# Optimization experiments

Measured on AMD Instinct MI355X. Metric: run time of the kernel, lower is better.

The kernel has to match this reference:

```python
import jax, jax.numpy as jnp
import numpy as np

FP8_MAX = 448.0  # max normal for float8_e4m3fn
BLOCK = 128


def setup_inputs() -> dict:
    key = jax.random.key(0)
    k1, k2, k3 = jax.random.split(key, 3)
    B, S, D_IN, D_OUT = 2, 2048, 4096, 8192
    x = jax.random.normal(k1, (B, S, D_IN), dtype=jnp.float32)
    # stored weight is fp8_e4m3fn; materialize as f32 values that are exactly fp8-representable
    w = jax.random.normal(k2, (D_OUT, D_IN), dtype=jnp.float32)
    weight = w.astype(jnp.float8_e4m3fn).astype(jnp.float32)
    # positive per-(128x128)-block dequant scales
    weight_scale_inv = (
        jax.random.uniform(k3, (D_OUT // BLOCK, D_IN // BLOCK), dtype=jnp.float32) * 0.05 + 0.005
    )
    return {"x": x, "weight": weight, "weight_scale_inv": weight_scale_inv}


def _quantize_per_token(x2d):
    # x2d: [M, K] -> fp8 values + [M, 1] f32 scale
    amax = jnp.clip(jnp.max(jnp.abs(x2d), axis=-1, keepdims=True), min=1e-12)
    x_scale = (amax / FP8_MAX).astype(jnp.float32)
    x_fp8 = (x2d / x_scale).astype(jnp.float8_e4m3fn)
    return x_fp8, x_scale


def _dequantize_weight(weight, weight_scale_inv):
    # weight: [O, K] (fp8-representable f32), scales: [O/B, K/B]
    O, K = weight.shape
    w_fp8 = weight.astype(jnp.float8_e4m3fn).astype(jnp.float32)
    wb = w_fp8.reshape(O // BLOCK, BLOCK, K // BLOCK, BLOCK)
    wb = wb * weight_scale_inv[:, None, :, None]
    return wb.reshape(O, K)


def reference(x, weight, weight_scale_inv):
    orig_shape = x.shape
    x2d = x.reshape(-1, orig_shape[-1])  # [M, K], M > 1 path
    x_fp8, x_scale = _quantize_per_token(x2d)
    # block-scaled fp8 GEMM: y[m,n] = x_scale[m] * sum_k x_fp8[m,k] * w_fp8[n,k] * s[n//B,k//B]
    w_deq = _dequantize_weight(weight, weight_scale_inv)  # [O, K]
    y = jnp.einsum("mk,ok->mo", x_fp8.astype(jnp.float32), w_deq) * x_scale
    return y.reshape(*orig_shape[:-1], weight.shape[0])
```

## Files before the change

kernel.cpp:

```cpp
#include <hip/hip_runtime.h>

typedef float f32x4  __attribute__((ext_vector_type(4)));
typedef float f32x16 __attribute__((ext_vector_type(16)));
typedef int   i32x4  __attribute__((ext_vector_type(4)));
typedef int   i32x8  __attribute__((ext_vector_type(8)));

#define AS1 __attribute__((address_space(1)))
#define AS3 __attribute__((address_space(3)))

__global__ __launch_bounds__(256) void quant_x_fp8_kernel(
    const float* __restrict__ x, unsigned char* __restrict__ x8,
    float* __restrict__ xs, int K) {
  int m = blockIdx.x;
  int t = threadIdx.x;
  const f32x4* src = (const f32x4*)(x + (size_t)m * K + t * 16);
  f32x4 v[4];
  float am = 0.0f;
#pragma unroll
  for (int i = 0; i < 4; ++i) {
    v[i] = src[i];
#pragma unroll
    for (int j = 0; j < 4; ++j) am = fmaxf(am, __builtin_fabsf(v[i][j]));
  }
#pragma unroll
  for (int off = 32; off >= 1; off >>= 1)
    am = fmaxf(am, __shfl_xor(am, off, 64));
  __shared__ float red[4];
  int wv = t >> 6, lane = t & 63;
  if (lane == 0) red[wv] = am;
  __syncthreads();
  am = fmaxf(fmaxf(red[0], red[1]), fmaxf(red[2], red[3]));
  am = fmaxf(am, 1e-12f);
  float sc = am / 448.0f;
  if (t == 0) xs[m] = sc;
  i32x4 out;
#pragma unroll
  for (int i = 0; i < 4; ++i) {
    float q0 = v[i][0] / sc, q1 = v[i][1] / sc;
    float q2 = v[i][2] / sc, q3 = v[i][3] / sc;
    int p = __builtin_amdgcn_cvt_pk_fp8_f32(q0, q1, 0, false);
    p = __builtin_amdgcn_cvt_pk_fp8_f32(q2, q3, p, true);
    out[i] = p;
  }
  *(i32x4*)(x8 + (size_t)m * K + t * 16) = out;
}

__global__ __launch_bounds__(256) void quant_w_fp8_kernel(
    const float* __restrict__ w, unsigned char* __restrict__ w8) {
  size_t idx = (size_t)blockIdx.x * 256 + threadIdx.x;
  const f32x4* src = (const f32x4*)w + idx * 4;
  i32x4 out;
#pragma unroll
  for (int i = 0; i < 4; ++i) {
    f32x4 v = src[i];
    int p = __builtin_amdgcn_cvt_pk_fp8_f32(v[0], v[1], 0, false);
    p = __builtin_amdgcn_cvt_pk_fp8_f32(v[2], v[3], p, true);
    out[i] = p;
  }
  ((i32x4*)w8)[idx] = out;
}

__global__ __launch_bounds__(512, 1) void gemm_mxfp8_kernel(
    const unsigned char* __restrict__ A8,
    const unsigned char* __restrict__ W8,
    const float* __restrict__ xs,
    const float* __restrict__ wsinv,
    float* __restrict__ Y,
    int M, int N, int K) {
  const int KB = K >> 7;

  int bid = blockIdx.x, nwg = gridDim.x;
  int wg = (bid & 7) * (nwg >> 3) + (bid >> 3);
  int mt = M >> 8;
  int bm = wg & (mt - 1);
  int bn = wg / mt;
  int m0 = bm << 8, n0 = bn << 7;

  __shared__ __align__(16) char lds[147456];

  const int tid = threadIdx.x, wv = tid >> 6, lane = tid & 63;
  const int wr = wv >> 1, wc = wv & 1;
  const int l31 = lane & 31, hi2 = lane >> 5;
  const int salt = l31 & 7;

  const int sL0 = ((hi2 * 2 + 0) ^ salt) << 4;
  const int sH0 = ((hi2 * 2 + 1) ^ salt) << 4;
  const int sL1 = ((4 + hi2 * 2 + 0) ^ salt) << 4;
  const int sH1 = ((4 + hi2 * 2 + 1) ^ salt) << 4;

  const int aRow = (wr * 64 + l31) * 128;
  const int bRow = (wc * 64 + l31) * 128;
  const int aL0 = aRow + sL0, aH0 = aRow + sH0;
  const int aL1 = aRow + sL1, aH1 = aRow + sH1;
  const int bL0 = bRow + sL0, bH0 = bRow + sH0;
  const int bL1 = bRow + sL1, bH1 = bRow + sH1;

  const int stgD = tid << 4;
  const int rIdx = tid >> 3;
  const int cSrc = ((tid & 7) ^ ((tid >> 3) & 7)) << 4;
  const size_t rowB = (size_t)K;
  const size_t g64 = 64 * rowB;
  const char* pA = (const char*)A8 + (size_t)(m0 + rIdx) * rowB + cSrc;
  const char* pB = (const char*)W8 + (size_t)(n0 + rIdx) * rowB + cSrc;

  const float* wsv = wsinv + (size_t)bn * KB;

  f32x16 acc[2][2];
#pragma unroll
  for (int i = 0; i < 2; ++i)
#pragma unroll
    for (int j = 0; j < 2; ++j) acc[i][j] = (f32x16)0.0f;

  i32x8 af[2], bf[2][2];

#define GL(SRC, DST)                                                           \
  __builtin_amdgcn_global_load_lds((const AS1 void*)(SRC), (AS3 void*)(DST),   \
                                   16, 0, 0)
#define STG_A(COND, SB, SRC)                                                   \
  if (COND) {                                                                  \
    const char* s_ = (SRC);                                                    \
    char* d_ = lds + (SB) + stgD;                                              \
    GL(s_, d_);                                                                \
    GL(s_ + g64, d_ + 8192);                                                   \
    GL(s_ + 2 * g64, d_ + 16384);                                              \
    GL(s_ + 3 * g64, d_ + 24576);                                              \
  }
#define STG_B(COND, SB, SRC)                                                   \
  if (COND) {                                                                  \
    const char* s_ = (SRC);                                                    \
    char* d_ = lds + (SB) + stgD;                                              \
    GL(s_, d_);                                                                \
    GL(s_ + g64, d_ + 8192);                                                   \
  }

#define RD_A(RB, MJ)                                                           \
  {                                                                            \
    const char* p_ = lds + (RB) + (MJ) * 4096;                                 \
    i32x4 lo0 = *(const i32x4*)(p_ + aL0);                                     \
    i32x4 hi0 = *(const i32x4*)(p_ + aH0);                                     \
    i32x4 lo1 = *(const i32x4*)(p_ + aL1);                                     \
    i32x4 hi1 = *(const i32x4*)(p_ + aH1);                                     \
    af[0] = __builtin_shufflevector(lo0, hi0, 0, 1, 2, 3, 4, 5, 6, 7);         \
    af[1] = __builtin_shufflevector(lo1, hi1, 0, 1, 2, 3, 4, 5, 6, 7);         \
  }
#define RD_Bn(RB, NJ)                                                          \
  {                                                                            \
    const char* p_ = lds + (RB) + (NJ) * 4096;                                 \
    i32x4 lo0 = *(const i32x4*)(p_ + bL0);                                     \
    i32x4 hi0 = *(const i32x4*)(p_ + bH0);                                     \
    i32x4 lo1 = *(const i32x4*)(p_ + bL1);                                     \
    i32x4 hi1 = *(const i32x4*)(p_ + bH1);                                     \
    bf[NJ][0] = __builtin_shufflevector(lo0, hi0, 0, 1, 2, 3, 4, 5, 6, 7);     \
    bf[NJ][1] = __builtin_shufflevector(lo1, hi1, 0, 1, 2, 3, 4, 5, 6, 7);     \
  }

#define MMFn(MJ, NJ, R_)                                                       \
  {                                                                            \
    _Pragma("unroll") for (int q = 0; q < 16; ++q)                             \
        acc[MJ][NJ][q] *= (R_);                                                \
    acc[MJ][NJ] = __builtin_amdgcn_mfma_scale_f32_32x32x64_f8f6f4(             \
        af[0], bf[NJ][0], acc[MJ][NJ], 0, 0, 0, 0x7f7f7f7f, 0, 0x7f7f7f7f);    \
    acc[MJ][NJ] = __builtin_amdgcn_mfma_scale_f32_32x32x64_f8f6f4(             \
        af[1], bf[NJ][1], acc[MJ][NJ], 0, 0, 0, 0x7f7f7f7f, 0, 0x7f7f7f7f);    \
  }

  STG_A(true, 0, pA);
  STG_B(true, 98304, pB);
  STG_A(true, 32768, pA + 128);
  STG_B(true, 114688, pB + 128);
  asm volatile("s_waitcnt vmcnt(6)" ::: "memory");
  __builtin_amdgcn_s_barrier();

  int rdA = 0;
  int stA = 65536;
  int rdB = 98304;
  int stB = 131072;
  const char* pAs = pA + 256;
  const char* pBs = pB + 256;
  float sp_ = wsv[0];

#define TILE(T, G, VM)                                                         \
  {                                                                            \
    float sc_ = wsv[(T)];                                                      \
    float r_ = sp_ / sc_;                                                      \
    RD_A(rdA, 0);                                                              \
    RD_Bn(rdB, 0);                                                             \
    __builtin_amdgcn_s_setprio(1);                                             \
    MMFn(0, 0, r_);                                                            \
    __builtin_amdgcn_s_setprio(0);                                             \
    STG_A(G, stA, pAs);                                                        \
    STG_B(G, stB, pBs);                                                        \
    RD_Bn(rdB, 1);                                                             \
    __builtin_amdgcn_s_setprio(1);                                             \
    MMFn(0, 1, r_);                                                            \
    __builtin_amdgcn_s_setprio(0);                                             \
    RD_A(rdA, 1);                                                              \
    __builtin_amdgcn_s_setprio(1);                                             \
    MMFn(1, 0, r_);                                                            \
    MMFn(1, 1, r_);                                                            \
    __builtin_amdgcn_s_setprio(0);                                             \
    sp_ = sc_;                                                                 \
    asm volatile("s_waitcnt " VM ::: "memory");                                \
    __builtin_amdgcn_s_barrier();                                              \
    rdA = (rdA == 65536) ? 0 : rdA + 32768;                                    \
    stA = (stA == 65536) ? 0 : stA + 32768;                                    \
    rdB = (rdB == 131072) ? 98304 : rdB + 16384;                               \
    stB = (stB == 131072) ? 98304 : stB + 16384;                               \
    pAs += 128;                                                                \
    pBs += 128;                                                                \
  }

#pragma unroll 1
  for (int t = 0; t < KB - 2; ++t) {
    TILE(t, true, "vmcnt(6)")
  }
  TILE(KB - 2, false, "vmcnt(0)")
  TILE(KB - 1, false, "vmcnt(0)")

#undef TILE
#undef MMFn
#undef RD_Bn
#undef RD_A
#undef STG_B
#undef STG_A
#undef GL

  const float sl_ = sp_;
#pragma unroll
  for (int mj = 0; mj < 2; ++mj)
#pragma unroll
    for (int nj = 0; nj < 2; ++nj) {
      int col = n0 + wc * 64 + nj * 32 + l31;
#pragma unroll
      for (int q = 0; q < 4; ++q) {
        int row0 = m0 + wr * 64 + mj * 32 + q * 8 + hi2 * 4;
        f32x4 sv = *(const f32x4*)(xs + row0);
#pragma unroll
        for (int j = 0; j < 4; ++j)
          Y[(size_t)(row0 + j) * N + col] = acc[mj][nj][q * 4 + j] * sv[j] * sl_;
      }
    }
}

extern "C" void kernel_launch(void* const* d_in, const int* in_sizes, int n_in,
                              void* d_out, int out_size, void* d_ws, size_t ws_size,
                              hipStream_t stream) {
  const float* x     = (const float*)d_in[0];
  const float* w     = (const float*)d_in[1];
  const float* wsinv = (const float*)d_in[2];
  float* y = (float*)d_out;

  const int K = 4096;
  const int M = in_sizes[0] / K;
  const int N = in_sizes[1] / K;

  unsigned char* x8 = (unsigned char*)d_ws;
  float* xs = (float*)((char*)d_ws + (size_t)M * K);
  unsigned char* w8 =
      (unsigned char*)d_ws + (size_t)M * K + (size_t)M * 4;

  quant_x_fp8_kernel<<<M, 256, 0, stream>>>(x, x8, xs, K);
  quant_w_fp8_kernel<<<(int)(((size_t)N * K / 16 + 255) / 256), 256, 0,
                       stream>>>(w, w8);

  dim3 grid((M / 256) * (N / 128));
  gemm_mxfp8_kernel<<<grid, 512, 0, stream>>>(x8, w8, xs, wsinv, y, M, N, K);
}
```

Before: 226.7 us.

## Shrink GEMM LDS pipeline to double-buffered A and single-buffered B

Replaces the 3-stage A / 3-stage B LDS ring buffer with a 2-stage A buffer and a single B buffer. B is now read fully up front and refilled after a mid-tile barrier. This cuts LDS use from 144KB to 80KB and raises the launch-bounds occupancy hint, which lets the kernel rely on more resident waves instead of deep prefetch. In exchange, prefetch depth drops, waits become vmcnt(0) every tile, and an extra barrier is added per k-block. Latency exposure may rise, and at 80KB of LDS per 512-thread block occupancy may still be limited.

```diff
diff --git a/kernel.cpp b/kernel.cpp
--- a/kernel.cpp
+++ b/kernel.cpp
@@ -60,7 +60,7 @@
   ((i32x4*)w8)[idx] = out;
 }
 
-__global__ __launch_bounds__(512, 1) void gemm_mxfp8_kernel(
+__global__ __launch_bounds__(512, 4) void gemm_mxfp8_kernel(
     const unsigned char* __restrict__ A8,
     const unsigned char* __restrict__ W8,
     const float* __restrict__ xs,
@@ -76,7 +76,7 @@
   int bn = wg / mt;
   int m0 = bm << 8, n0 = bn << 7;
 
-  __shared__ __align__(16) char lds[147456];
+  __shared__ __align__(16) char lds[81920];
 
   const int tid = threadIdx.x, wv = tid >> 6, lane = tid & 63;
   const int wr = wv >> 1, wc = wv & 1;
@@ -143,15 +143,15 @@
     af[0] = __builtin_shufflevector(lo0, hi0, 0, 1, 2, 3, 4, 5, 6, 7);         \
     af[1] = __builtin_shufflevector(lo1, hi1, 0, 1, 2, 3, 4, 5, 6, 7);         \
   }
-#define RD_Bn(RB, NJ)                                                          \
-  {                                                                            \
-    const char* p_ = lds + (RB) + (NJ) * 4096;                                 \
+#define RD_B(BR)                                                               \
+  _Pragma("unroll") for (int nj = 0; nj < 2; ++nj) {                           \
+    const char* p_ = lds + (BR) + nj * 4096;                                   \
     i32x4 lo0 = *(const i32x4*)(p_ + bL0);                                     \
     i32x4 hi0 = *(const i32x4*)(p_ + bH0);                                     \
     i32x4 lo1 = *(const i32x4*)(p_ + bL1);                                     \
     i32x4 hi1 = *(const i32x4*)(p_ + bH1);                                     \
-    bf[NJ][0] = __builtin_shufflevector(lo0, hi0, 0, 1, 2, 3, 4, 5, 6, 7);     \
-    bf[NJ][1] = __builtin_shufflevector(lo1, hi1, 0, 1, 2, 3, 4, 5, 6, 7);     \
+    bf[nj][0] = __builtin_shufflevector(lo0, hi0, 0, 1, 2, 3, 4, 5, 6, 7);     \
+    bf[nj][1] = __builtin_shufflevector(lo1, hi1, 0, 1, 2, 3, 4, 5, 6, 7);     \
   }
 
 #define MMFn(MJ, NJ, R_)                                                       \
@@ -165,32 +165,28 @@
   }
 
   STG_A(true, 0, pA);
-  STG_B(true, 98304, pB);
-  STG_A(true, 32768, pA + 128);
-  STG_B(true, 114688, pB + 128);
-  asm volatile("s_waitcnt vmcnt(6)" ::: "memory");
+  STG_B(true, 65536, pB);
+  asm volatile("s_waitcnt vmcnt(0)" ::: "memory");
   __builtin_amdgcn_s_barrier();
 
-  int rdA = 0;
-  int stA = 65536;
-  int rdB = 98304;
-  int stB = 131072;
-  const char* pAs = pA + 256;
-  const char* pBs = pB + 256;
+  int rdA = 0, stA = 32768;
+  const char* pAs = pA + 128;
+  const char* pBs = pB + 128;
   float sp_ = wsv[0];
 
-#define TILE(T, G, VM)                                                         \
+#define TILE(T, G)                                                             \
   {                                                                            \
     float sc_ = wsv[(T)];                                                      \
     float r_ = sp_ / sc_;                                                      \
+    RD_B(65536);                                                               \
     RD_A(rdA, 0);                                                              \
-    RD_Bn(rdB, 0);                                                             \
+    STG_A(G, stA, pAs);                                                        \
     __builtin_amdgcn_s_setprio(1);                                             \
     MMFn(0, 0, r_);                                                            \
     __builtin_amdgcn_s_setprio(0);                                             \
-    STG_A(G, stA, pAs);                                                        \
-    STG_B(G, stB, pBs);                                                        \
-    RD_Bn(rdB, 1);                                                             \
+    asm volatile("s_waitcnt lgkmcnt(0)" ::: "memory");                         \
+    __builtin_amdgcn_s_barrier();                                              \
+    STG_B(G, 65536, pBs);                                                      \
     __builtin_amdgcn_s_setprio(1);                                             \
     MMFn(0, 1, r_);                                                            \
     __builtin_amdgcn_s_setprio(0);                                             \
@@ -200,26 +196,23 @@
     MMFn(1, 1, r_);                                                            \
     __builtin_amdgcn_s_setprio(0);                                             \
     sp_ = sc_;                                                                 \
-    asm volatile("s_waitcnt " VM ::: "memory");                                \
+    asm volatile("s_waitcnt vmcnt(0)" ::: "memory");                           \
     __builtin_amdgcn_s_barrier();                                              \
-    rdA = (rdA == 65536) ? 0 : rdA + 32768;                                    \
-    stA = (stA == 65536) ? 0 : stA + 32768;                                    \
-    rdB = (rdB == 131072) ? 98304 : rdB + 16384;                               \
-    stB = (stB == 131072) ? 98304 : stB + 16384;                               \
+    rdA ^= 32768;                                                              \
+    stA ^= 32768;                                                              \
     pAs += 128;                                                                \
     pBs += 128;                                                                \
   }
 
 #pragma unroll 1
-  for (int t = 0; t < KB - 2; ++t) {
-    TILE(t, true, "vmcnt(6)")
-  }
-  TILE(KB - 2, false, "vmcnt(0)")
-  TILE(KB - 1, false, "vmcnt(0)")
+  for (int t = 0; t < KB - 1; ++t) {
+    TILE(t, true)
+  }
+  TILE(KB - 1, false)
 
 #undef TILE
 #undef MMFn
-#undef RD_Bn
+#undef RD_B
 #undef RD_A
 #undef STG_B
 #undef STG_A
```

New measurement: 824.0 us. +263.6%, slower.

## Halve workgroup to 4 waves with 128x64 per-wave tiles and triple-buffered LDS

Applied to the files above, without the earlier changes.

The GEMM now runs 256 threads (4 waves) per workgroup instead of 512. Each wave computes a 128x64 output tile (4x2 MFMA blocks) instead of 64x64, which raises register reuse of the B fragments per LDS read. The LDS layout changes to three interleaved A+B stage buffers of 48KB each, and the global-to-LDS load issue is spread across the tile's MFMA groups. The trade-off is more accumulator registers per wave and half as many waves to hide latency.

```diff
diff --git a/kernel.cpp b/kernel.cpp
--- a/kernel.cpp
+++ b/kernel.cpp
@@ -60,7 +60,7 @@
   ((i32x4*)w8)[idx] = out;
 }
 
-__global__ __launch_bounds__(512, 1) void gemm_mxfp8_kernel(
+__global__ __launch_bounds__(256, 1) void gemm_mxfp8_kernel(
     const unsigned char* __restrict__ A8,
     const unsigned char* __restrict__ W8,
     const float* __restrict__ xs,
@@ -88,7 +88,7 @@
   const int sL1 = ((4 + hi2 * 2 + 0) ^ salt) << 4;
   const int sH1 = ((4 + hi2 * 2 + 1) ^ salt) << 4;
 
-  const int aRow = (wr * 64 + l31) * 128;
+  const int aRow = (wr * 128 + l31) * 128;
   const int bRow = (wc * 64 + l31) * 128;
   const int aL0 = aRow + sL0, aH0 = aRow + sH0;
   const int aL1 = aRow + sL1, aH1 = aRow + sH1;
@@ -97,17 +97,17 @@
 
   const int stgD = tid << 4;
   const int rIdx = tid >> 3;
-  const int cSrc = ((tid & 7) ^ ((tid >> 3) & 7)) << 4;
+  const int cSrc = ((tid & 7) ^ (rIdx & 7)) << 4;
   const size_t rowB = (size_t)K;
-  const size_t g64 = 64 * rowB;
+  const size_t g32 = 32 * rowB;
   const char* pA = (const char*)A8 + (size_t)(m0 + rIdx) * rowB + cSrc;
   const char* pB = (const char*)W8 + (size_t)(n0 + rIdx) * rowB + cSrc;
 
   const float* wsv = wsinv + (size_t)bn * KB;
 
-  f32x16 acc[2][2];
-#pragma unroll
-  for (int i = 0; i < 2; ++i)
+  f32x16 acc[4][2];
+#pragma unroll
+  for (int i = 0; i < 4; ++i)
 #pragma unroll
     for (int j = 0; j < 2; ++j) acc[i][j] = (f32x16)0.0f;
 
@@ -121,16 +121,22 @@
     const char* s_ = (SRC);                                                    \
     char* d_ = lds + (SB) + stgD;                                              \
     GL(s_, d_);                                                                \
-    GL(s_ + g64, d_ + 8192);                                                   \
-    GL(s_ + 2 * g64, d_ + 16384);                                              \
-    GL(s_ + 3 * g64, d_ + 24576);                                              \
+    GL(s_ + g32, d_ + 4096);                                                   \
+    GL(s_ + 2 * g32, d_ + 8192);                                               \
+    GL(s_ + 3 * g32, d_ + 12288);                                              \
+    GL(s_ + 4 * g32, d_ + 16384);                                              \
+    GL(s_ + 5 * g32, d_ + 20480);                                              \
+    GL(s_ + 6 * g32, d_ + 24576);                                              \
+    GL(s_ + 7 * g32, d_ + 28672);                                              \
   }
 #define STG_B(COND, SB, SRC)                                                   \
   if (COND) {                                                                  \
     const char* s_ = (SRC);                                                    \
-    char* d_ = lds + (SB) + stgD;                                              \
+    char* d_ = lds + (SB) + 32768 + stgD;                                      \
     GL(s_, d_);                                                                \
-    GL(s_ + g64, d_ + 8192);                                                   \
+    GL(s_ + g32, d_ + 4096);                                                   \
+    GL(s_ + 2 * g32, d_ + 8192);                                               \
+    GL(s_ + 3 * g32, d_ + 12288);                                              \
   }
 
 #define RD_A(RB, MJ)                                                           \
@@ -143,15 +149,15 @@
     af[0] = __builtin_shufflevector(lo0, hi0, 0, 1, 2, 3, 4, 5, 6, 7);         \
     af[1] = __builtin_shufflevector(lo1, hi1, 0, 1, 2, 3, 4, 5, 6, 7);         \
   }
-#define RD_Bn(RB, NJ)                                                          \
-  {                                                                            \
-    const char* p_ = lds + (RB) + (NJ) * 4096;                                 \
+#define RD_B(RB)                                                               \
+  _Pragma("unroll") for (int nj = 0; nj < 2; ++nj) {                           \
+    const char* p_ = lds + (RB) + 32768 + nj * 4096;                           \
     i32x4 lo0 = *(const i32x4*)(p_ + bL0);                                     \
     i32x4 hi0 = *(const i32x4*)(p_ + bH0);                                     \
     i32x4 lo1 = *(const i32x4*)(p_ + bL1);                                     \
     i32x4 hi1 = *(const i32x4*)(p_ + bH1);                                     \
-    bf[NJ][0] = __builtin_shufflevector(lo0, hi0, 0, 1, 2, 3, 4, 5, 6, 7);     \
-    bf[NJ][1] = __builtin_shufflevector(lo1, hi1, 0, 1, 2, 3, 4, 5, 6, 7);     \
+    bf[nj][0] = __builtin_shufflevector(lo0, hi0, 0, 1, 2, 3, 4, 5, 6, 7);     \
+    bf[nj][1] = __builtin_shufflevector(lo1, hi1, 0, 1, 2, 3, 4, 5, 6, 7);     \
   }
 
 #define MMFn(MJ, NJ, R_)                                                       \
@@ -165,16 +171,13 @@
   }
 
   STG_A(true, 0, pA);
-  STG_B(true, 98304, pB);
-  STG_A(true, 32768, pA + 128);
-  STG_B(true, 114688, pB + 128);
-  asm volatile("s_waitcnt vmcnt(6)" ::: "memory");
+  STG_B(true, 0, pB);
+  STG_A(true, 49152, pA + 128);
+  STG_B(true, 49152, pB + 128);
+  asm volatile("s_waitcnt vmcnt(12)" ::: "memory");
   __builtin_amdgcn_s_barrier();
 
-  int rdA = 0;
-  int stA = 65536;
-  int rdB = 98304;
-  int stB = 131072;
+  int rdT = 0, stT = 98304;
   const char* pAs = pA + 256;
   const char* pBs = pB + 256;
   float sp_ = wsv[0];
@@ -183,43 +186,48 @@
   {                                                                            \
     float sc_ = wsv[(T)];                                                      \
     float r_ = sp_ / sc_;                                                      \
-    RD_A(rdA, 0);                                                              \
-    RD_Bn(rdB, 0);                                                             \
+    RD_B(rdT);                                                                 \
+    RD_A(rdT, 0);                                                              \
     __builtin_amdgcn_s_setprio(1);                                             \
     MMFn(0, 0, r_);                                                            \
-    __builtin_amdgcn_s_setprio(0);                                             \
-    STG_A(G, stA, pAs);                                                        \
-    STG_B(G, stB, pBs);                                                        \
-    RD_Bn(rdB, 1);                                                             \
-    __builtin_amdgcn_s_setprio(1);                                             \
     MMFn(0, 1, r_);                                                            \
     __builtin_amdgcn_s_setprio(0);                                             \
-    RD_A(rdA, 1);                                                              \
+    STG_A(G, stT, pAs);                                                        \
+    RD_A(rdT, 1);                                                              \
     __builtin_amdgcn_s_setprio(1);                                             \
     MMFn(1, 0, r_);                                                            \
     MMFn(1, 1, r_);                                                            \
+    __builtin_amdgcn_s_setprio(0);                                             \
+    STG_B(G, stT, pBs);                                                        \
+    RD_A(rdT, 2);                                                              \
+    __builtin_amdgcn_s_setprio(1);                                             \
+    MMFn(2, 0, r_);                                                            \
+    MMFn(2, 1, r_);                                                            \
+    __builtin_amdgcn_s_setprio(0);                                             \
+    RD_A(rdT, 3);                                                              \
+    __builtin_amdgcn_s_setprio(1);                                             \
+    MMFn(3, 0, r_);                                                            \
+    MMFn(3, 1, r_);                                                            \
     __builtin_amdgcn_s_setprio(0);                                             \
     sp_ = sc_;                                                                 \
     asm volatile("s_waitcnt " VM ::: "memory");                                \
     __builtin_amdgcn_s_barrier();                                              \
-    rdA = (rdA == 65536) ? 0 : rdA + 32768;                                    \
-    stA = (stA == 65536) ? 0 : stA + 32768;                                    \
-    rdB = (rdB == 131072) ? 98304 : rdB + 16384;                               \
-    stB = (stB == 131072) ? 98304 : stB + 16384;                               \
+    rdT = (rdT == 98304) ? 0 : rdT + 49152;                                    \
+    stT = (stT == 98304) ? 0 : stT + 49152;                                    \
     pAs += 128;                                                                \
     pBs += 128;                                                                \
   }
 
 #pragma unroll 1
   for (int t = 0; t < KB - 2; ++t) {
-    TILE(t, true, "vmcnt(6)")
+    TILE(t, true, "vmcnt(12)")
   }
   TILE(KB - 2, false, "vmcnt(0)")
   TILE(KB - 1, false, "vmcnt(0)")
 
 #undef TILE
 #undef MMFn
-#undef RD_Bn
+#undef RD_B
 #undef RD_A
 #undef STG_B
 #undef STG_A
@@ -227,13 +235,13 @@
 
   const float sl_ = sp_;
 #pragma unroll
-  for (int mj = 0; mj < 2; ++mj)
+  for (int mj = 0; mj < 4; ++mj)
 #pragma unroll
     for (int nj = 0; nj < 2; ++nj) {
       int col = n0 + wc * 64 + nj * 32 + l31;
 #pragma unroll
       for (int q = 0; q < 4; ++q) {
-        int row0 = m0 + wr * 64 + mj * 32 + q * 8 + hi2 * 4;
+        int row0 = m0 + wr * 128 + mj * 32 + q * 8 + hi2 * 4;
         f32x4 sv = *(const f32x4*)(xs + row0);
 #pragma unroll
         for (int j = 0; j < 4; ++j)
@@ -264,5 +272,5 @@
                        stream>>>(w, w8);
 
   dim3 grid((M / 256) * (N / 128));
-  gemm_mxfp8_kernel<<<grid, 512, 0, stream>>>(x8, w8, xs, wsinv, y, M, N, K);
-}
+  gemm_mxfp8_kernel<<<grid, 256, 0, stream>>>(x8, w8, xs, wsinv, y, M, N, K);
+}
```

Measured after the change: 275.1 us. 1.21x slower.
